# Kernel optimization log

Measured on AMD Instinct MI355X. Metric: run time of the kernel, lower is better.

Reference implementation:

```python
import jax, jax.numpy as jnp
import numpy as np

B, S, H = 2, 1024, 4096
NH, NKV, HD = 32, 8, 128
GROUPS = NH // NKV  # num_key_value_groups
ROPE_THETA = 10000.0


def setup_inputs() -> dict:
    key = jax.random.key(0)
    k0, k1, k2 = jax.random.split(key, 3)
    x = jax.random.normal(k0, (B, S, H), jnp.float32)
    w_qkv = jax.random.normal(k1, (H, (NH + 2 * NKV) * HD), jnp.float32) * (1.0 / np.sqrt(H))
    w_o = jax.random.normal(k2, (NH * HD, H), jnp.float32) * (1.0 / np.sqrt(H))
    # rotary cos/sin tables (llama freqs_cis, interleaved-pair convention)
    inv_freq = 1.0 / (ROPE_THETA ** (np.arange(0, HD, 2, dtype=np.float64) / HD))
    freqs = np.outer(np.arange(S, dtype=np.float64), inv_freq)  # [S, HD/2]
    cos = jnp.asarray(np.cos(freqs), jnp.float32)
    sin = jnp.asarray(np.sin(freqs), jnp.float32)
    # additive causal mask [1,1,S,S]
    causal = np.tril(np.ones((S, S), dtype=bool))
    mask = jnp.asarray(np.where(causal, 0.0, -1e9), jnp.float32)[None, None]
    return {"x": x, "w_qkv": w_qkv, "w_o": w_o, "cos": cos, "sin": sin, "mask": mask}


def _rope(t, cos, sin):
    # t: [B,S,N,HD]; rotate interleaved (even, odd) pairs like complex mult by freqs_cis
    t2 = t.reshape(t.shape[:-1] + (HD // 2, 2))
    t0, t1 = t2[..., 0], t2[..., 1]
    c = cos[None, :, None, :]  # [1,S,1,HD/2]
    s = sin[None, :, None, :]
    r0 = t0 * c - t1 * s
    r1 = t0 * s + t1 * c
    return jnp.stack([r0, r1], axis=-1).reshape(t.shape)


def reference(x, w_qkv, w_o, cos, sin, mask):
    b, s, _ = x.shape
    xqkv = (x @ w_qkv).reshape(b, s, NH + 2 * NKV, HD)
    xq = xqkv[:, :, :NH]                  # [b,s,NH,HD]
    xk = xqkv[:, :, NH:NH + NKV]          # [b,s,NKV,HD]
    xv = xqkv[:, :, NH + NKV:]            # [b,s,NKV,HD]
    xq = _rope(xq, cos, sin)
    xk = _rope(xk, cos, sin)
    # GQA: repeat kv heads to match query heads (repeat_interleave on head dim)
    k = jnp.repeat(xk, GROUPS, axis=2)
    v = jnp.repeat(xv, GROUPS, axis=2)
    scores = jnp.einsum('bqhd,bkhd->bhqk', xq, k) / np.float32(np.sqrt(HD))
    scores = scores + mask
    probs = jax.nn.softmax(scores.astype(jnp.float32), axis=-1).astype(xq.dtype)
    out = jnp.einsum('bhqk,bkhd->bqhd', probs, v).reshape(b, s, NH * HD)
    return out @ w_o
```

## Files before the change

### kernel.cpp

```cpp
#include <hip/hip_runtime.h>
#include <cstdint>
#include <cstddef>

typedef short bf16x8 __attribute__((ext_vector_type(8)));
typedef float f32x4 __attribute__((ext_vector_type(4)));

__device__ __forceinline__ unsigned short f2bf(float f) {
  unsigned int u = __builtin_bit_cast(unsigned int, f);
  u += 0x7fffu + ((u >> 16) & 1u);
  return (unsigned short)(u >> 16);
}

__global__ void k_convert(const float* __restrict__ in, unsigned short* __restrict__ out, int n4) {
  int i = blockIdx.x * blockDim.x + threadIdx.x;
  if (i >= n4) return;
  float4 v = ((const float4*)in)[i];
  ushort4 o;
  o.x = f2bf(v.x); o.y = f2bf(v.y); o.z = f2bf(v.z); o.w = f2bf(v.w);
  ((ushort4*)out)[i] = o;
}

__global__ void k_transpose(const float* __restrict__ src, unsigned short* __restrict__ dst,
                            int K, int N) {
  __shared__ float t[32][33];
  int n0 = blockIdx.x * 32, k0 = blockIdx.y * 32;
  int tx = threadIdx.x, ty = threadIdx.y;
#pragma unroll
  for (int i = 0; i < 4; ++i)
    t[ty * 4 + i][tx] = src[(size_t)(k0 + ty * 4 + i) * N + n0 + tx];
  __syncthreads();
#pragma unroll
  for (int i = 0; i < 4; ++i)
    dst[(size_t)(n0 + ty * 4 + i) * K + k0 + tx] = f2bf(t[tx][ty * 4 + i]);
}

__global__ __launch_bounds__(256) void k_gemm(const unsigned short* __restrict__ A,
                                              const unsigned short* __restrict__ Bt,
                                              float* __restrict__ C, int M, int N, int K) {
  __shared__ __align__(16) unsigned short lA[128 * 64];
  __shared__ __align__(16) unsigned short lB[128 * 64];
  const int tid = threadIdx.x;
  const int lane = tid & 63, wv = tid >> 6;
  const int wr = wv >> 1, wc = wv & 1;
  const int bm = blockIdx.x * 128, bn = blockIdx.y * 128;
  const int l16 = lane & 15, lhi = lane >> 4;
  f32x4 acc[4][4] = {};
  bf16x8 ar[4], br[4];

#pragma unroll
  for (int i = 0; i < 4; ++i) {
    int c = tid + i * 256, row = c >> 3, c16 = c & 7;
    ar[i] = *(const bf16x8*)(A + (size_t)(bm + row) * K + 0 + c16 * 8);
    br[i] = *(const bf16x8*)(Bt + (size_t)(bn + row) * K + 0 + c16 * 8);
  }
  const int nkt = K >> 6;
  for (int kt = 0; kt < nkt; ++kt) {
    __syncthreads();
#pragma unroll
    for (int i = 0; i < 4; ++i) {
      int c = tid + i * 256, row = c >> 3, c16 = c & 7;
      int pc = c16 ^ (row & 7);
      *(bf16x8*)((char*)lA + row * 128 + pc * 16) = ar[i];
      *(bf16x8*)((char*)lB + row * 128 + pc * 16) = br[i];
    }
    __syncthreads();
    if (kt + 1 < nkt) {
      int kofs = (kt + 1) << 6;
#pragma unroll
      for (int i = 0; i < 4; ++i) {
        int c = tid + i * 256, row = c >> 3, c16 = c & 7;
        ar[i] = *(const bf16x8*)(A + (size_t)(bm + row) * K + kofs + c16 * 8);
        br[i] = *(const bf16x8*)(Bt + (size_t)(bn + row) * K + kofs + c16 * 8);
      }
    }
#pragma unroll
    for (int s = 0; s < 2; ++s) {
      bf16x8 af[4], bfr[4];
#pragma unroll
      for (int f = 0; f < 4; ++f) {
        int rowa = wr * 64 + f * 16 + l16;
        int ca = (s * 4 + lhi) ^ (rowa & 7);
        af[f] = *(const bf16x8*)((char*)lA + rowa * 128 + ca * 16);
        int rowb = wc * 64 + f * 16 + l16;
        int cb = (s * 4 + lhi) ^ (rowb & 7);
        bfr[f] = *(const bf16x8*)((char*)lB + rowb * 128 + cb * 16);
      }
#pragma unroll
      for (int fi = 0; fi < 4; ++fi)
#pragma unroll
        for (int fj = 0; fj < 4; ++fj)
          acc[fi][fj] = __builtin_amdgcn_mfma_f32_16x16x32_bf16(af[fi], bfr[fj], acc[fi][fj], 0, 0, 0);
    }
  }
#pragma unroll
  for (int fi = 0; fi < 4; ++fi) {
    int rbase = bm + wr * 64 + fi * 16 + lhi * 4;
#pragma unroll
    for (int fj = 0; fj < 4; ++fj) {
      int col = bn + wc * 64 + fj * 16 + l16;
#pragma unroll
      for (int r = 0; r < 4; ++r)
        C[(size_t)(rbase + r) * N + col] = acc[fi][fj][r];
    }
  }
}

__global__ void k_rope(const float* __restrict__ xqkv, const float* __restrict__ cosT,
                       const float* __restrict__ sinT, unsigned short* __restrict__ Qr,
                       unsigned short* __restrict__ Kr) {
  int bs = blockIdx.x;
  int b = bs >> 10, s = bs & 1023;
  int head = blockIdx.y * 4 + (threadIdx.x >> 6);
  int i = threadIdx.x & 63;
  const float* src = xqkv + ((size_t)bs * 48 + head) * 128 + i * 2;
  float2 t = *(const float2*)src;
  float c = cosT[s * 64 + i], sn = sinT[s * 64 + i];
  float r0 = t.x * c - t.y * sn;
  float r1 = t.x * sn + t.y * c;
  unsigned int packed = (unsigned int)f2bf(r0) | ((unsigned int)f2bf(r1) << 16);
  if (head < 32) {
    *(unsigned int*)(Qr + (((size_t)(b * 32 + head) * 1024 + s) * 128 + i * 2)) = packed;
  } else {
    int kvh = head - 32;
    *(unsigned int*)(Kr + (((size_t)(b * 8 + kvh) * 1024 + s) * 128 + i * 2)) = packed;
  }
}

__global__ void k_vt(const float* __restrict__ xqkv, unsigned short* __restrict__ Vt) {
  __shared__ float t[32][33];
  int s0 = blockIdx.x * 32, d0 = blockIdx.y * 32;
  int bk = blockIdx.z;
  int tx = threadIdx.x, ty = threadIdx.y;
  int b = bk >> 3, kvh = bk & 7;
#pragma unroll
  for (int i = 0; i < 4; ++i)
    t[ty * 4 + i][tx] =
        xqkv[(((size_t)(b * 1024 + s0 + ty * 4 + i)) * 48 + 40 + kvh) * 128 + d0 + tx];
  __syncthreads();
#pragma unroll
  for (int i = 0; i < 4; ++i)
    Vt[((size_t)bk * 128 + d0 + ty * 4 + i) * 1024 + s0 + tx] = f2bf(t[tx][ty * 4 + i]);
}

__global__ __launch_bounds__(256) void k_attn(const unsigned short* __restrict__ Qr,
                                              const unsigned short* __restrict__ Kr,
                                              const unsigned short* __restrict__ Vt,
                                              unsigned short* __restrict__ Out) {
  __shared__ __align__(16) unsigned short lK[64 * 128];
  __shared__ __align__(16) unsigned short lV[128 * 64];
  __shared__ __align__(16) unsigned short lP[4 * 16 * 64];
  const int tid = threadIdx.x, lane = tid & 63, wv = tid >> 6;
  const int qt = blockIdx.x, h = blockIdx.y, b = blockIdx.z;
  const int kvh = h >> 2;
  const int q0 = qt * 64;
  const int l16 = lane & 15, lhi = lane >> 4;

  const unsigned short* Qbase = Qr + ((size_t)(b * 32 + h) * 1024 + q0 + wv * 16 + l16) * 128;
  bf16x8 qf[4];
#pragma unroll
  for (int s = 0; s < 4; ++s) qf[s] = *(const bf16x8*)(Qbase + s * 32 + lhi * 8);

  const unsigned short* Kbase = Kr + (size_t)(b * 8 + kvh) * 1024 * 128;
  const unsigned short* Vbase = Vt + (size_t)(b * 8 + kvh) * 128 * 1024;

  f32x4 oacc[8] = {};
  float mrow[4] = {-1e30f, -1e30f, -1e30f, -1e30f};
  float lrow[4] = {0.f, 0.f, 0.f, 0.f};
  const int ntk = qt + 1;
  bf16x8 kreg[4], vreg[4];

  for (int kt = 0; kt < ntk; ++kt) {
    const int k0 = kt * 64;
#pragma unroll
    for (int i = 0; i < 4; ++i) {
      int c = tid + i * 256;
      int krow = c >> 4, kc = c & 15;
      kreg[i] = *(const bf16x8*)(Kbase + (size_t)(k0 + krow) * 128 + kc * 8);
      int vrow = c >> 3, vc = c & 7;
      vreg[i] = *(const bf16x8*)(Vbase + (size_t)vrow * 1024 + k0 + vc * 8);
    }
    __syncthreads();
#pragma unroll
    for (int i = 0; i < 4; ++i) {
      int c = tid + i * 256;
      int krow = c >> 4, kc = c & 15;
      *(bf16x8*)((char*)lK + krow * 256 + (kc ^ (krow & 7)) * 16) = kreg[i];
      int vrow = c >> 3, vc = c & 7;
      *(bf16x8*)((char*)lV + vrow * 128 + (vc ^ (vrow & 7)) * 16) = vreg[i];
    }
    __syncthreads();

    f32x4 sacc[4] = {};
#pragma unroll
    for (int kf = 0; kf < 4; ++kf) {
      int rowk = kf * 16 + l16;
#pragma unroll
      for (int s = 0; s < 4; ++s) {
        int ck = (s * 4 + lhi) ^ (rowk & 7);
        bf16x8 kfr = *(const bf16x8*)((char*)lK + rowk * 256 + ck * 16);
        sacc[kf] = __builtin_amdgcn_mfma_f32_16x16x32_bf16(qf[s], kfr, sacc[kf], 0, 0, 0);
      }
    }

    const int qg = q0 + wv * 16 + lhi * 4;
    float mt[4] = {-1e30f, -1e30f, -1e30f, -1e30f};
#pragma unroll
    for (int kf = 0; kf < 4; ++kf) {
      int kg = k0 + kf * 16 + l16;
#pragma unroll
      for (int r = 0; r < 4; ++r) {
        float v = sacc[kf][r] * 0.08838834764831845f;
        v = (kg <= qg + r) ? v : -1e9f;
        sacc[kf][r] = v;
        mt[r] = fmaxf(mt[r], v);
      }
    }
#pragma unroll
    for (int r = 0; r < 4; ++r) {
#pragma unroll
      for (int off = 1; off < 16; off <<= 1) mt[r] = fmaxf(mt[r], __shfl_xor(mt[r], off));
    }
    float alpha[4], rs[4];
#pragma unroll
    for (int r = 0; r < 4; ++r) {
      float mn = fmaxf(mrow[r], mt[r]);
      alpha[r] = __expf(mrow[r] - mn);
      mrow[r] = mn;
      rs[r] = 0.f;
    }
#pragma unroll
    for (int kf = 0; kf < 4; ++kf) {
      int key = kf * 16 + l16;
#pragma unroll
      for (int r = 0; r < 4; ++r) {
        float p = __expf(sacc[kf][r] - mrow[r]);
        rs[r] += p;
        int prow = lhi * 4 + r;
        int addr = wv * 2048 + ((prow * 128 + key * 2) ^ ((prow & 7) << 4));
        *(unsigned short*)((char*)lP + addr) = f2bf(p);
      }
    }
#pragma unroll
    for (int r = 0; r < 4; ++r) {
#pragma unroll
      for (int off = 1; off < 16; off <<= 1) rs[r] += __shfl_xor(rs[r], off);
      lrow[r] = lrow[r] * alpha[r] + rs[r];
    }
#pragma unroll
    for (int nf = 0; nf < 8; ++nf)
#pragma unroll
      for (int r = 0; r < 4; ++r) oacc[nf][r] *= alpha[r];

#pragma unroll
    for (int s2 = 0; s2 < 2; ++s2) {
      int prow = l16;
      int paddr = wv * 2048 + ((prow * 128 + s2 * 64 + lhi * 16) ^ ((prow & 7) << 4));
      bf16x8 pa = *(const bf16x8*)((char*)lP + paddr);
#pragma unroll
      for (int nf = 0; nf < 8; ++nf) {
        int rowd = nf * 16 + l16;
        int cv = (s2 * 4 + lhi) ^ (rowd & 7);
        bf16x8 vfr = *(const bf16x8*)((char*)lV + rowd * 128 + cv * 16);
        oacc[nf] = __builtin_amdgcn_mfma_f32_16x16x32_bf16(pa, vfr, oacc[nf], 0, 0, 0);
      }
    }
  }

  unsigned short* Ob = Out + ((size_t)(b * 1024) + q0 + wv * 16 + lhi * 4) * 4096 + h * 128;
#pragma unroll
  for (int r = 0; r < 4; ++r) {
    float inv = 1.f / lrow[r];
#pragma unroll
    for (int nf = 0; nf < 8; ++nf)
      Ob[(size_t)r * 4096 + nf * 16 + l16] = f2bf(oacc[nf][r] * inv);
  }
}

extern "C" void kernel_launch(void* const* d_in, const int* in_sizes, int n_in,
                              void* d_out, int out_size, void* d_ws, size_t ws_size,
                              hipStream_t stream) {
  const float* x = (const float*)d_in[0];
  const float* w_qkv = (const float*)d_in[1];
  const float* w_o = (const float*)d_in[2];
  const float* cosT = (const float*)d_in[3];
  const float* sinT = (const float*)d_in[4];

  char* ws = (char*)d_ws;
  unsigned short* wqkv_t = (unsigned short*)(ws);
  unsigned short* wo_t   = (unsigned short*)(ws + 50331648);
  unsigned short* xb     = (unsigned short*)(ws + 83886080);
  float*          xqkv   = (float*)(ws + 100663296);
  unsigned short* attn   = (unsigned short*)(ws + 100663296);
  unsigned short* Qr     = (unsigned short*)(ws + 150994944);
  unsigned short* Kr     = (unsigned short*)(ws + 167772160);
  unsigned short* Vt     = (unsigned short*)(ws + 171966464);

  k_convert<<<8192, 256, 0, stream>>>(x, xb, 2048 * 4096 / 4);
  k_transpose<<<dim3(6144 / 32, 4096 / 32), dim3(32, 8), 0, stream>>>(w_qkv, wqkv_t, 4096, 6144);
  k_transpose<<<dim3(4096 / 32, 4096 / 32), dim3(32, 8), 0, stream>>>(w_o, wo_t, 4096, 4096);
  k_gemm<<<dim3(16, 48), 256, 0, stream>>>(xb, wqkv_t, xqkv, 2048, 6144, 4096);
  k_rope<<<dim3(2048, 10), 256, 0, stream>>>(xqkv, cosT, sinT, Qr, Kr);
  k_vt<<<dim3(32, 4, 16), dim3(32, 8), 0, stream>>>(xqkv, Vt);
  k_attn<<<dim3(16, 32, 2), 256, 0, stream>>>(Qr, Kr, Vt, attn);
  k_gemm<<<dim3(16, 32), 256, 0, stream>>>(attn, wo_t, (float*)d_out, 2048, 4096, 4096);
}
```

Before: 349.3 us.

## Fuse RoPE and V-transpose into QKV GEMM epilogue; use direct global-to-LDS loads

The QKV GEMM now applies rotary embedding and writes bf16 Q/K and transposed V directly in its epilogue, which removes the fp32 xqkv round trip and the separate rope and V-transpose kernels. The GEMM main loop now uses global_load_lds to fill shared memory directly. This drops the register prefetch double-buffering and the XOR swizzle, so the LDS fragment reads may hit bank conflicts and global latency is no longer overlapped with compute. Attention now reads K and V fragments straight from global memory instead of staging them in LDS, which relies on cache hits and may increase memory traffic.

Result: slower. 555.3 us (+59.0%).

```diff
diff --git a/kernel.cpp b/kernel.cpp
--- a/kernel.cpp
+++ b/kernel.cpp
@@ -4,11 +4,18 @@
 
 typedef short bf16x8 __attribute__((ext_vector_type(8)));
 typedef float f32x4 __attribute__((ext_vector_type(4)));
+typedef unsigned short ushort_t;
 
 __device__ __forceinline__ unsigned short f2bf(float f) {
   unsigned int u = __builtin_bit_cast(unsigned int, f);
   u += 0x7fffu + ((u >> 16) & 1u);
   return (unsigned short)(u >> 16);
+}
+
+__device__ __forceinline__ void gload_lds(const unsigned short* g, unsigned short* l) {
+  __builtin_amdgcn_global_load_lds(
+      (const __attribute__((address_space(1))) unsigned int*)g,
+      (__attribute__((address_space(3))) unsigned int*)l, 16, 0, 0);
 }
 
 __global__ void k_convert(const float* __restrict__ in, unsigned short* __restrict__ out, int n4) {
@@ -34,9 +41,16 @@
     dst[(size_t)(n0 + ty * 4 + i) * K + k0 + tx] = f2bf(t[tx][ty * 4 + i]);
 }
 
+template <int MODE>
 __global__ __launch_bounds__(256) void k_gemm(const unsigned short* __restrict__ A,
                                               const unsigned short* __restrict__ Bt,
-                                              float* __restrict__ C, int M, int N, int K) {
+                                              float* __restrict__ C,
+                                              unsigned short* __restrict__ Qr,
+                                              unsigned short* __restrict__ Kr,
+                                              unsigned short* __restrict__ Vt,
+                                              const float* __restrict__ cosT,
+                                              const float* __restrict__ sinT,
+                                              int M, int N, int K) {
   __shared__ __align__(16) unsigned short lA[128 * 64];
   __shared__ __align__(16) unsigned short lB[128 * 64];
   const int tid = threadIdx.x;
@@ -44,46 +58,27 @@
   const int wr = wv >> 1, wc = wv & 1;
   const int bm = blockIdx.x * 128, bn = blockIdx.y * 128;
   const int l16 = lane & 15, lhi = lane >> 4;
+  const int lrow = lane >> 3, lchunk = lane & 7;
   f32x4 acc[4][4] = {};
-  bf16x8 ar[4], br[4];
-
-#pragma unroll
-  for (int i = 0; i < 4; ++i) {
-    int c = tid + i * 256, row = c >> 3, c16 = c & 7;
-    ar[i] = *(const bf16x8*)(A + (size_t)(bm + row) * K + 0 + c16 * 8);
-    br[i] = *(const bf16x8*)(Bt + (size_t)(bn + row) * K + 0 + c16 * 8);
-  }
+
   const int nkt = K >> 6;
   for (int kt = 0; kt < nkt; ++kt) {
+    const int k0 = kt << 6;
     __syncthreads();
 #pragma unroll
-    for (int i = 0; i < 4; ++i) {
-      int c = tid + i * 256, row = c >> 3, c16 = c & 7;
-      int pc = c16 ^ (row & 7);
-      *(bf16x8*)((char*)lA + row * 128 + pc * 16) = ar[i];
-      *(bf16x8*)((char*)lB + row * 128 + pc * 16) = br[i];
+    for (int j = 0; j < 4; ++j) {
+      int row = wv * 32 + j * 8 + lrow;
+      gload_lds(A + (size_t)(bm + row) * K + k0 + lchunk * 8, lA + (wv * 32 + j * 8) * 64);
+      gload_lds(Bt + (size_t)(bn + row) * K + k0 + lchunk * 8, lB + (wv * 32 + j * 8) * 64);
     }
     __syncthreads();
-    if (kt + 1 < nkt) {
-      int kofs = (kt + 1) << 6;
-#pragma unroll
-      for (int i = 0; i < 4; ++i) {
-        int c = tid + i * 256, row = c >> 3, c16 = c & 7;
-        ar[i] = *(const bf16x8*)(A + (size_t)(bm + row) * K + kofs + c16 * 8);
-        br[i] = *(const bf16x8*)(Bt + (size_t)(bn + row) * K + kofs + c16 * 8);
-      }
-    }
 #pragma unroll
     for (int s = 0; s < 2; ++s) {
       bf16x8 af[4], bfr[4];
 #pragma unroll
       for (int f = 0; f < 4; ++f) {
-        int rowa = wr * 64 + f * 16 + l16;
-        int ca = (s * 4 + lhi) ^ (rowa & 7);
-        af[f] = *(const bf16x8*)((char*)lA + rowa * 128 + ca * 16);
-        int rowb = wc * 64 + f * 16 + l16;
-        int cb = (s * 4 + lhi) ^ (rowb & 7);
-        bfr[f] = *(const bf16x8*)((char*)lB + rowb * 128 + cb * 16);
+        af[f] = *(const bf16x8*)(lA + (wr * 64 + f * 16 + l16) * 64 + (s * 4 + lhi) * 8);
+        bfr[f] = *(const bf16x8*)(lB + (wc * 64 + f * 16 + l16) * 64 + (s * 4 + lhi) * 8);
       }
 #pragma unroll
       for (int fi = 0; fi < 4; ++fi)
@@ -92,62 +87,58 @@
           acc[fi][fj] = __builtin_amdgcn_mfma_f32_16x16x32_bf16(af[fi], bfr[fj], acc[fi][fj], 0, 0, 0);
     }
   }
-#pragma unroll
-  for (int fi = 0; fi < 4; ++fi) {
-    int rbase = bm + wr * 64 + fi * 16 + lhi * 4;
-#pragma unroll
-    for (int fj = 0; fj < 4; ++fj) {
-      int col = bn + wc * 64 + fj * 16 + l16;
-#pragma unroll
-      for (int r = 0; r < 4; ++r)
-        C[(size_t)(rbase + r) * N + col] = acc[fi][fj][r];
-    }
-  }
-}
-
-__global__ void k_rope(const float* __restrict__ xqkv, const float* __restrict__ cosT,
-                       const float* __restrict__ sinT, unsigned short* __restrict__ Qr,
-                       unsigned short* __restrict__ Kr) {
-  int bs = blockIdx.x;
-  int b = bs >> 10, s = bs & 1023;
-  int head = blockIdx.y * 4 + (threadIdx.x >> 6);
-  int i = threadIdx.x & 63;
-  const float* src = xqkv + ((size_t)bs * 48 + head) * 128 + i * 2;
-  float2 t = *(const float2*)src;
-  float c = cosT[s * 64 + i], sn = sinT[s * 64 + i];
-  float r0 = t.x * c - t.y * sn;
-  float r1 = t.x * sn + t.y * c;
-  unsigned int packed = (unsigned int)f2bf(r0) | ((unsigned int)f2bf(r1) << 16);
-  if (head < 32) {
-    *(unsigned int*)(Qr + (((size_t)(b * 32 + head) * 1024 + s) * 128 + i * 2)) = packed;
+
+  if (MODE == 0) {
+#pragma unroll
+    for (int fi = 0; fi < 4; ++fi) {
+      int rbase = bm + wr * 64 + fi * 16 + lhi * 4;
+#pragma unroll
+      for (int fj = 0; fj < 4; ++fj) {
+        int col = bn + wc * 64 + fj * 16 + l16;
+#pragma unroll
+        for (int r = 0; r < 4; ++r)
+          C[(size_t)(rbase + r) * N + col] = acc[fi][fj][r];
+      }
+    }
   } else {
-    int kvh = head - 32;
-    *(unsigned int*)(Kr + (((size_t)(b * 8 + kvh) * 1024 + s) * 128 + i * 2)) = packed;
-  }
-}
-
-__global__ void k_vt(const float* __restrict__ xqkv, unsigned short* __restrict__ Vt) {
-  __shared__ float t[32][33];
-  int s0 = blockIdx.x * 32, d0 = blockIdx.y * 32;
-  int bk = blockIdx.z;
-  int tx = threadIdx.x, ty = threadIdx.y;
-  int b = bk >> 3, kvh = bk & 7;
-#pragma unroll
-  for (int i = 0; i < 4; ++i)
-    t[ty * 4 + i][tx] =
-        xqkv[(((size_t)(b * 1024 + s0 + ty * 4 + i)) * 48 + 40 + kvh) * 128 + d0 + tx];
-  __syncthreads();
-#pragma unroll
-  for (int i = 0; i < 4; ++i)
-    Vt[((size_t)bk * 128 + d0 + ty * 4 + i) * 1024 + s0 + tx] = f2bf(t[tx][ty * 4 + i]);
+#pragma unroll
+    for (int fi = 0; fi < 4; ++fi) {
+      int rbase = bm + wr * 64 + fi * 16 + lhi * 4;
+      int b = rbase >> 10, sbase = rbase & 1023;
+#pragma unroll
+      for (int fj = 0; fj < 4; ++fj) {
+        int col = bn + wc * 64 + fj * 16 + l16;
+        if (col < 5120) {
+          int i = (col & 127) >> 1;
+          float sgn = (col & 1) ? 1.0f : -1.0f;
+          unsigned short* dst;
+          if (col < 4096)
+            dst = Qr + ((size_t)(b * 32 + (col >> 7)) * 1024) * 128 + (col & 127);
+          else
+            dst = Kr + ((size_t)(b * 8 + ((col - 4096) >> 7)) * 1024) * 128 + (col & 127);
+#pragma unroll
+          for (int r = 0; r < 4; ++r) {
+            float own = acc[fi][fj][r];
+            float other = __shfl_xor(own, 1);
+            int s = sbase + r;
+            float c = cosT[s * 64 + i], sn = sinT[s * 64 + i];
+            dst[(size_t)s * 128] = f2bf(own * c + sgn * other * sn);
+          }
+        } else {
+          int kvh = (col - 5120) >> 7, d = col & 127;
+          unsigned short* dst = Vt + ((size_t)(b * 8 + kvh) * 128 + d) * 1024;
+#pragma unroll
+          for (int r = 0; r < 4; ++r) dst[sbase + r] = f2bf(acc[fi][fj][r]);
+        }
+      }
+    }
+  }
 }
 
 __global__ __launch_bounds__(256) void k_attn(const unsigned short* __restrict__ Qr,
                                               const unsigned short* __restrict__ Kr,
                                               const unsigned short* __restrict__ Vt,
                                               unsigned short* __restrict__ Out) {
-  __shared__ __align__(16) unsigned short lK[64 * 128];
-  __shared__ __align__(16) unsigned short lV[128 * 64];
   __shared__ __align__(16) unsigned short lP[4 * 16 * 64];
   const int tid = threadIdx.x, lane = tid & 63, wv = tid >> 6;
   const int qt = blockIdx.x, h = blockIdx.y, b = blockIdx.z;
@@ -167,37 +158,17 @@
   float mrow[4] = {-1e30f, -1e30f, -1e30f, -1e30f};
   float lrow[4] = {0.f, 0.f, 0.f, 0.f};
   const int ntk = qt + 1;
-  bf16x8 kreg[4], vreg[4];
 
   for (int kt = 0; kt < ntk; ++kt) {
     const int k0 = kt * 64;
-#pragma unroll
-    for (int i = 0; i < 4; ++i) {
-      int c = tid + i * 256;
-      int krow = c >> 4, kc = c & 15;
-      kreg[i] = *(const bf16x8*)(Kbase + (size_t)(k0 + krow) * 128 + kc * 8);
-      int vrow = c >> 3, vc = c & 7;
-      vreg[i] = *(const bf16x8*)(Vbase + (size_t)vrow * 1024 + k0 + vc * 8);
-    }
-    __syncthreads();
-#pragma unroll
-    for (int i = 0; i < 4; ++i) {
-      int c = tid + i * 256;
-      int krow = c >> 4, kc = c & 15;
-      *(bf16x8*)((char*)lK + krow * 256 + (kc ^ (krow & 7)) * 16) = kreg[i];
-      int vrow = c >> 3, vc = c & 7;
-      *(bf16x8*)((char*)lV + vrow * 128 + (vc ^ (vrow & 7)) * 16) = vreg[i];
-    }
-    __syncthreads();
 
     f32x4 sacc[4] = {};
 #pragma unroll
     for (int kf = 0; kf < 4; ++kf) {
-      int rowk = kf * 16 + l16;
+      const unsigned short* Krow = Kbase + (size_t)(k0 + kf * 16 + l16) * 128;
 #pragma unroll
       for (int s = 0; s < 4; ++s) {
-        int ck = (s * 4 + lhi) ^ (rowk & 7);
-        bf16x8 kfr = *(const bf16x8*)((char*)lK + rowk * 256 + ck * 16);
+        bf16x8 kfr = *(const bf16x8*)(Krow + (s * 4 + lhi) * 8);
         sacc[kf] = __builtin_amdgcn_mfma_f32_16x16x32_bf16(qf[s], kfr, sacc[kf], 0, 0, 0);
       }
     }
@@ -253,14 +224,11 @@
 
 #pragma unroll
     for (int s2 = 0; s2 < 2; ++s2) {
-      int prow = l16;
-      int paddr = wv * 2048 + ((prow * 128 + s2 * 64 + lhi * 16) ^ ((prow & 7) << 4));
+      int paddr = wv * 2048 + ((l16 * 128 + s2 * 64 + lhi * 16) ^ ((l16 & 7) << 4));
       bf16x8 pa = *(const bf16x8*)((char*)lP + paddr);
 #pragma unroll
       for (int nf = 0; nf < 8; ++nf) {
-        int rowd = nf * 16 + l16;
-        int cv = (s2 * 4 + lhi) ^ (rowd & 7);
-        bf16x8 vfr = *(const bf16x8*)((char*)lV + rowd * 128 + cv * 16);
+        bf16x8 vfr = *(const bf16x8*)(Vbase + (size_t)(nf * 16 + l16) * 1024 + k0 + (s2 * 4 + lhi) * 8);
         oacc[nf] = __builtin_amdgcn_mfma_f32_16x16x32_bf16(pa, vfr, oacc[nf], 0, 0, 0);
       }
     }
@@ -289,18 +257,17 @@
   unsigned short* wqkv_t = (unsigned short*)(ws);
   unsigned short* wo_t   = (unsigned short*)(ws + 50331648);
   unsigned short* xb     = (unsigned short*)(ws + 83886080);
-  float*          xqkv   = (float*)(ws + 100663296);
-  unsigned short* attn   = (unsigned short*)(ws + 100663296);
-  unsigned short* Qr     = (unsigned short*)(ws + 150994944);
-  unsigned short* Kr     = (unsigned short*)(ws + 167772160);
-  unsigned short* Vt     = (unsigned short*)(ws + 171966464);
+  unsigned short* Qr     = (unsigned short*)(ws + 100663296);
+  unsigned short* Kr     = (unsigned short*)(ws + 117440512);
+  unsigned short* Vt     = (unsigned short*)(ws + 121634816);
+  unsigned short* attn   = (unsigned short*)(ws + 125829120);
 
   k_convert<<<8192, 256, 0, stream>>>(x, xb, 2048 * 4096 / 4);
   k_transpose<<<dim3(6144 / 32, 4096 / 32), dim3(32, 8), 0, stream>>>(w_qkv, wqkv_t, 4096, 6144);
   k_transpose<<<dim3(4096 / 32, 4096 / 32), dim3(32, 8), 0, stream>>>(w_o, wo_t, 4096, 4096);
-  k_gemm<<<dim3(16, 48), 256, 0, stream>>>(xb, wqkv_t, xqkv, 2048, 6144, 4096);
-  k_rope<<<dim3(2048, 10), 256, 0, stream>>>(xqkv, cosT, sinT, Qr, Kr);
-  k_vt<<<dim3(32, 4, 16), dim3(32, 8), 0, stream>>>(xqkv, Vt);
+  k_gemm<1><<<dim3(16, 48), 256, 0, stream>>>(xb, wqkv_t, nullptr, Qr, Kr, Vt, cosT, sinT,
+                                              2048, 6144, 4096);
   k_attn<<<dim3(16, 32, 2), 256, 0, stream>>>(Qr, Kr, Vt, attn);
-  k_gemm<<<dim3(16, 32), 256, 0, stream>>>(attn, wo_t, (float*)d_out, 2048, 4096, 4096);
-}
+  k_gemm<0><<<dim3(16, 32), 256, 0, stream>>>(attn, wo_t, (float*)d_out, nullptr, nullptr, nullptr,
+                                              nullptr, nullptr, 2048, 4096, 4096);
+}
```
